# Performance work log

Hardware: AMD Instinct MI355X
Metric: run time of the kernel (lower is better)

Reference implementation:

```python
import jax, jax.numpy as jnp
import numpy as np

N_ATOMS = 100_000
N_BONDS = 200_000
MAX_NB = 6
ATOM_FDIM = 133
BOND_FDIM = 147
HIDDEN = 256
DEPTH = 5
ATOMS_PER_MOL = 100


def setup_inputs() -> dict:
    key = jax.random.key(0)
    ks = jax.random.split(key, 9)
    f_atoms = jax.random.normal(ks[0], (N_ATOMS, ATOM_FDIM), dtype=jnp.float32)
    f_bonds = jax.random.normal(ks[1], (N_BONDS, BOND_FDIM), dtype=jnp.float32)
    a2b = jax.random.randint(ks[2], (N_ATOMS, MAX_NB), 0, N_BONDS, dtype=jnp.int32)
    b2a = jax.random.randint(ks[3], (N_BONDS,), 0, N_ATOMS, dtype=jnp.int32)
    # reverse bond of 2i is 2i+1 and vice versa (chemprop directed-bond pairing)
    b2revb = (jnp.arange(N_BONDS, dtype=jnp.int32) ^ 1)
    s_i = 1.0 / np.sqrt(BOND_FDIM)
    s_h = 1.0 / np.sqrt(HIDDEN)
    s_o = 1.0 / np.sqrt(ATOM_FDIM + HIDDEN)
    W_i = jax.random.uniform(ks[4], (HIDDEN, BOND_FDIM), jnp.float32, -s_i, s_i)
    W_h = jax.random.uniform(ks[5], (HIDDEN, HIDDEN), jnp.float32, -s_h, s_h)
    W_o = jax.random.uniform(ks[6], (HIDDEN, ATOM_FDIM + HIDDEN), jnp.float32, -s_o, s_o)
    b_o = jax.random.uniform(ks[7], (HIDDEN,), jnp.float32, -s_o, s_o)
    return {"f_atoms": f_atoms, "f_bonds": f_bonds, "a2b": a2b, "b2a": b2a,
            "b2revb": b2revb, "W_i": W_i, "W_h": W_h, "W_o": W_o, "b_o": b_o,
            "atoms_per_mol": ATOMS_PER_MOL}


def reference(f_atoms, f_bonds, a2b, b2a, b2revb, W_i, W_h, W_o, b_o, atoms_per_mol):
    # input = W_i(f_bonds); message = relu(input)   [n_bonds, H]
    inp = jnp.einsum('bf,hf->bh', f_bonds, W_i)
    message = jax.nn.relu(inp)
    for _ in range(DEPTH - 1):
        # gather incoming-bond messages per atom and sum: [n_atoms, max_nb, H] -> [n_atoms, H]
        a_message = message[a2b].sum(axis=1)
        # directed-MPNN update: subtract reverse-bond message
        m = a_message[b2a] - message[b2revb]
        message = jax.nn.relu(inp + jnp.einsum('bh,gh->bg', m, W_h))
        # dropout p=0.0 (eval) -> identity
    a_message = message[a2b].sum(axis=1)                      # [n_atoms, H]
    a_input = jnp.concatenate([f_atoms, a_message], axis=1)   # [n_atoms, atom_fdim+H]
    atom_hiddens = jax.nn.relu(jnp.einsum('af,hf->ah', a_input, W_o) + b_o)
    # uniform a_scope: stack per-molecule atom blocks -> [n_mols, atoms_per_mol, H]
    return atom_hiddens.reshape(-1, atoms_per_mol, HIDDEN)
```

## Files before the change

kernel.cpp:

```cpp
#include <hip/hip_runtime.h>
#include <hip/hip_bf16.h>

typedef unsigned short u16;
typedef unsigned short u16x8 __attribute__((ext_vector_type(8)));
typedef short s8vec __attribute__((ext_vector_type(8)));
typedef float f4vec __attribute__((ext_vector_type(4)));

__device__ __forceinline__ float bf2f(u16 u) {
    union { unsigned int i; float f; } c; c.i = ((unsigned int)u) << 16; return c.f;
}
__device__ __forceinline__ u16 f2bf(float f) {
    union { float f; unsigned int i; } c; c.f = f;
    unsigned int x = c.i;
    x += 0x7fffu + ((x >> 16) & 1u);
    return (u16)(x >> 16);
}

__device__ __forceinline__ void gload_lds16(const void* g, void* l) {
    __builtin_amdgcn_global_load_lds((__attribute__((address_space(1))) void*)g,
                                     (__attribute__((address_space(3))) void*)l, 16, 0, 0);
}

__global__ void pad_w_kernel(const float* __restrict__ src, u16* __restrict__ dst,
                             int sstride, int col0, int nvalid, int dcol) {
    int r = blockIdx.x;
    for (int c = threadIdx.x; c < dcol; c += blockDim.x) {
        float v = (c < nvalid) ? src[(size_t)r * sstride + col0 + c] : 0.f;
        dst[(size_t)r * dcol + c] = f2bf(v);
    }
}

__global__ void gather6_kernel(const u16* __restrict__ P, const int* __restrict__ a2b,
                               u16* __restrict__ out, int n_atoms) {
    int lane = threadIdx.x & 63;
    int half = lane >> 5;
    int col = (lane & 31) * 8;
    int wid = (blockIdx.x * blockDim.x + threadIdx.x) >> 6;
    int nw = (gridDim.x * blockDim.x) >> 6;
    for (int a0 = wid * 2; a0 < n_atoms; a0 += nw * 2) {
        int a = a0 + half;
        float acc[8];
#pragma unroll
        for (int e = 0; e < 8; ++e) acc[e] = 0.f;
#pragma unroll
        for (int j = 0; j < 6; ++j) {
            int b = a2b[a * 6 + j];
            u16x8 v = *(const u16x8*)(P + (size_t)b * 256 + col);
#pragma unroll
            for (int e = 0; e < 8; ++e) acc[e] += bf2f(v[e]);
        }
        u16x8 o;
#pragma unroll
        for (int e = 0; e < 8; ++e) o[e] = f2bf(acc[e]);
        *(u16x8*)(out + (size_t)a * 256 + col) = o;
    }
}

template <int ASTAGE, int EPI>
__launch_bounds__(512, 2)
__global__ void gemm256_kernel(const void* __restrict__ Asrc, const u16* __restrict__ Pm,
                               const u16* __restrict__ aPm, const int* __restrict__ b2a,
                               const u16* __restrict__ B, int M, int Kp, int scol, int nk,
                               void* __restrict__ out0, const u16* __restrict__ aQ,
                               const float* __restrict__ bias) {
    __shared__ __align__(16) char smem[2][49152];
    const int t = threadIdx.x;
    const int w = t >> 6, lane = t & 63;
    const int row0 = blockIdx.x * 128;
    const int wm = w >> 2, wn = w & 3;

    f4vec acc[4][4];
#pragma unroll
    for (int i = 0; i < 4; ++i)
#pragma unroll
        for (int j = 0; j < 4; ++j) acc[i][j] = (f4vec){0.f, 0.f, 0.f, 0.f};

    auto stage = [&](int buf, int k0) {
#pragma unroll
        for (int i = 0; i < 4; ++i) {
            int rlin = (w * 4 + i) * 8 + (lane >> 3);
            int slot = lane & 7;
            int chunk = slot ^ (rlin & 7);
            const u16* gp = B + (size_t)rlin * Kp + k0 + chunk * 8;
            gload_lds16(gp, &smem[buf][16384 + (w * 4 + i) * 1024]);
        }
#pragma unroll
        for (int i = 0; i < 2; ++i) {
            int cid = t * 2 + i;
            int r = cid >> 3, slot = cid & 7;
            int grow = row0 + r; if (grow >= M) grow = M - 1;
            int coff = k0 + slot * 8;
            u16x8 v;
            if (ASTAGE == 1) {
                const float* src = (const float*)Asrc + (size_t)grow * scol;
#pragma unroll
                for (int e = 0; e < 8; ++e) {
                    int c = coff + e;
                    v[e] = (c < scol) ? f2bf(src[c]) : (u16)0;
                }
            } else if (ASTAGE == 2) {
                u16x8 x = *(const u16x8*)((const u16*)Asrc + (size_t)grow * 256 + coff);
#pragma unroll
                for (int e = 0; e < 8; ++e) v[e] = (x[e] >> 15) ? (u16)0 : x[e];
            } else {
                int pr = grow ^ 1;
                int a = b2a[grow];
                u16x8 vi = *(const u16x8*)((const u16*)Asrc + (size_t)grow * 256 + coff);
                u16x8 vp = *(const u16x8*)(Pm + (size_t)pr * 256 + coff);
                u16x8 va = *(const u16x8*)(aPm + (size_t)a * 256 + coff);
#pragma unroll
                for (int e = 0; e < 8; ++e)
                    v[e] = f2bf(fmaxf(bf2f(vi[e]) + bf2f(va[e]) - bf2f(vp[e]), 0.f));
            }
            int chunk = slot ^ (r & 7);
            *(u16x8*)&smem[buf][r * 128 + chunk * 16] = v;
        }
    };

    auto compute = [&](int buf) {
#pragma unroll
        for (int kk = 0; kk < 2; ++kk) {
            s8vec af[4], bfr[4];
#pragma unroll
            for (int i = 0; i < 4; ++i) {
                int r = wm * 64 + i * 16 + (lane & 15);
                int chunk = (kk * 4 + (lane >> 4)) ^ (r & 7);
                af[i] = *(const s8vec*)&smem[buf][r * 128 + chunk * 16];
            }
#pragma unroll
            for (int j = 0; j < 4; ++j) {
                int c = wn * 64 + j * 16 + (lane & 15);
                int chunk = (kk * 4 + (lane >> 4)) ^ (c & 7);
                bfr[j] = *(const s8vec*)&smem[buf][16384 + c * 128 + chunk * 16];
            }
#pragma unroll
            for (int i = 0; i < 4; ++i)
#pragma unroll
                for (int j = 0; j < 4; ++j)
                    acc[i][j] = __builtin_amdgcn_mfma_f32_16x16x32_bf16(af[i], bfr[j], acc[i][j], 0, 0, 0);
        }
    };

    stage(0, 0);
    __syncthreads();
    int cur = 0;
    for (int ks = 0; ks < nk; ++ks) {
        if (ks + 1 < nk) stage(cur ^ 1, (ks + 1) * 64);
        compute(cur);
        __syncthreads();
        cur ^= 1;
    }

#pragma unroll
    for (int i = 0; i < 4; ++i) {
        int Rbase = row0 + wm * 64 + i * 16 + (lane >> 4) * 4;
#pragma unroll
        for (int j = 0; j < 4; ++j) {
            int C = wn * 64 + j * 16 + (lane & 15);
#pragma unroll
            for (int r = 0; r < 4; ++r) {
                int R = Rbase + r;
                if (R < M) {
                    float v = acc[i][j][r];
                    if (EPI == 0) {
                        ((u16*)out0)[(size_t)R * 256 + C] = f2bf(v);
                    } else {
                        float o = v + bf2f(aQ[(size_t)R * 256 + C]) + bias[C];
                        ((float*)out0)[(size_t)R * 256 + C] = fmaxf(o, 0.f);
                    }
                }
            }
        }
    }
}

extern "C" void kernel_launch(void* const* d_in, const int* in_sizes, int n_in,
                              void* d_out, int out_size, void* d_ws, size_t ws_size,
                              hipStream_t stream) {
    const float* f_atoms = (const float*)d_in[0];
    const float* f_bonds = (const float*)d_in[1];
    const int* a2b = (const int*)d_in[2];
    const int* b2a = (const int*)d_in[3];
    const float* W_i = (const float*)d_in[5];
    const float* W_h = (const float*)d_in[6];
    const float* W_o = (const float*)d_in[7];
    const float* b_o = (const float*)d_in[8];

    const int NA = 100000, NB = 200000;

    char* ws = (char*)d_ws;
    u16* inp = (u16*)(ws + 0);
    u16* Pa  = (u16*)(ws + 102400000);
    u16* Pb  = (u16*)(ws + 204800000);
    u16* aP  = (u16*)(ws + 307200000);
    u16* Wi  = (u16*)(ws + 358400000);
    u16* Wh  = (u16*)(ws + 358498304);
    u16* Wo2 = (u16*)(ws + 358629376);
    u16* Wo1 = (u16*)(ws + 358760448);
    if (ws_size < 358858752u) return;

    pad_w_kernel<<<dim3(256), dim3(256), 0, stream>>>(W_i, Wi, 147, 0, 147, 192);
    pad_w_kernel<<<dim3(256), dim3(256), 0, stream>>>(W_h, Wh, 256, 0, 256, 256);
    pad_w_kernel<<<dim3(256), dim3(256), 0, stream>>>(W_o, Wo2, 389, 133, 256, 256);
    pad_w_kernel<<<dim3(256), dim3(256), 0, stream>>>(W_o, Wo1, 389, 0, 133, 192);

    const int GB = (NB + 127) / 128;
    const int GA = (NA + 127) / 128;

    gemm256_kernel<1, 0><<<dim3(GB), dim3(512), 0, stream>>>(
        f_bonds, nullptr, nullptr, nullptr, Wi, NB, 192, 147, 3, inp, nullptr, nullptr);

    gemm256_kernel<2, 0><<<dim3(GB), dim3(512), 0, stream>>>(
        inp, nullptr, nullptr, nullptr, Wh, NB, 256, 0, 4, Pa, nullptr, nullptr);
    gather6_kernel<<<dim3(2048), dim3(256), 0, stream>>>(Pa, a2b, aP, NA);

    u16* Pcur = Pa; u16* Pnxt = Pb;
    for (int it = 0; it < 3; ++it) {
        gemm256_kernel<4, 0><<<dim3(GB), dim3(512), 0, stream>>>(
            inp, Pcur, aP, b2a, Wh, NB, 256, 0, 4, Pnxt, nullptr, nullptr);
        gather6_kernel<<<dim3(2048), dim3(256), 0, stream>>>(Pnxt, a2b, aP, NA);
        u16* tmp = Pcur; Pcur = Pnxt; Pnxt = tmp;
    }

    gemm256_kernel<4, 0><<<dim3(GB), dim3(512), 0, stream>>>(
        inp, Pcur, aP, b2a, Wo2, NB, 256, 0, 4, Pnxt, nullptr, nullptr);
    gather6_kernel<<<dim3(2048), dim3(256), 0, stream>>>(Pnxt, a2b, aP, NA);

    gemm256_kernel<1, 3><<<dim3(GA), dim3(512), 0, stream>>>(
        f_atoms, nullptr, nullptr, nullptr, Wo1, NA, 192, 133, 3, d_out, aP, b_o);
}
```

Before: 1.034 ms.

## Shrink GEMM tiles to 64 rows with K=32 steps and register-prefetched A

The GEMM block changes from 128 rows with 512 threads and K=64 steps to 64 rows with 256 threads and K=32 steps. LDS per block drops from 96KB to 40KB, so more blocks can be resident per CU. A-operand global loads are now issued into registers before the MFMA compute and written to LDS afterwards, overlapping load latency with math. The b2a lookup is hoisted out of the K loop, and the four weight-padding launches are merged into one. The risk is that smaller tiles reread the weight matrix twice as often and take more sync steps per tile.

```diff
diff --git a/kernel.cpp b/kernel.cpp
--- a/kernel.cpp
+++ b/kernel.cpp
@@ -15,15 +15,23 @@
     x += 0x7fffu + ((x >> 16) & 1u);
     return (u16)(x >> 16);
 }
-
 __device__ __forceinline__ void gload_lds16(const void* g, void* l) {
     __builtin_amdgcn_global_load_lds((__attribute__((address_space(1))) void*)g,
                                      (__attribute__((address_space(3))) void*)l, 16, 0, 0);
 }
-
-__global__ void pad_w_kernel(const float* __restrict__ src, u16* __restrict__ dst,
-                             int sstride, int col0, int nvalid, int dcol) {
+__device__ __forceinline__ int sw4(int r) { return (r + (r >> 2)) & 3; }
+
+__global__ void pad_w_all(const float* __restrict__ W_i, const float* __restrict__ W_h,
+                          const float* __restrict__ W_o,
+                          u16* __restrict__ Wi, u16* __restrict__ Wh,
+                          u16* __restrict__ Wo2, u16* __restrict__ Wo1) {
     int r = blockIdx.x;
+    int which = blockIdx.y;
+    const float* src; u16* dst; int sstride, col0, nvalid, dcol;
+    if (which == 0)      { src = W_i; dst = Wi;  sstride = 147; col0 = 0;   nvalid = 147; dcol = 192; }
+    else if (which == 1) { src = W_h; dst = Wh;  sstride = 256; col0 = 0;   nvalid = 256; dcol = 256; }
+    else if (which == 2) { src = W_o; dst = Wo2; sstride = 389; col0 = 133; nvalid = 256; dcol = 256; }
+    else                 { src = W_o; dst = Wo1; sstride = 389; col0 = 0;   nvalid = 133; dcol = 192; }
     for (int c = threadIdx.x; c < dcol; c += blockDim.x) {
         float v = (c < nvalid) ? src[(size_t)r * sstride + col0 + c] : 0.f;
         dst[(size_t)r * dcol + c] = f2bf(v);
@@ -57,17 +65,23 @@
 }
 
 template <int ASTAGE, int EPI>
-__launch_bounds__(512, 2)
+__launch_bounds__(256, 4)
 __global__ void gemm256_kernel(const void* __restrict__ Asrc, const u16* __restrict__ Pm,
                                const u16* __restrict__ aPm, const int* __restrict__ b2a,
-                               const u16* __restrict__ B, int M, int Kp, int scol, int nk,
+                               const u16* __restrict__ Bw, int M, int Kp, int scol, int nk,
                                void* __restrict__ out0, const u16* __restrict__ aQ,
                                const float* __restrict__ bias) {
-    __shared__ __align__(16) char smem[2][49152];
+    __shared__ __align__(16) char smem[2][20480];
     const int t = threadIdx.x;
     const int w = t >> 6, lane = t & 63;
-    const int row0 = blockIdx.x * 128;
-    const int wm = w >> 2, wn = w & 3;
+    const int row0 = blockIdx.x * 64;
+
+    const int ar = t >> 2;
+    const int aslot = t & 3;
+    int grow = row0 + ar; if (grow >= M) grow = M - 1;
+    const int aphys = aslot ^ sw4(ar);
+    int nbrow = 0;
+    if (ASTAGE == 4) nbrow = b2a[grow];
 
     f4vec acc[4][4];
 #pragma unroll
@@ -75,88 +89,91 @@
 #pragma unroll
         for (int j = 0; j < 4; ++j) acc[i][j] = (f4vec){0.f, 0.f, 0.f, 0.f};
 
-    auto stage = [&](int buf, int k0) {
+    u16x8 rv0, rv1, rv2;
+    float rs[8];
+
+    auto stageA_load = [&](int k0) {
+        int coff = k0 + aslot * 8;
+        if (ASTAGE == 1) {
+            const float* src = (const float*)Asrc + (size_t)grow * scol;
+#pragma unroll
+            for (int e = 0; e < 8; ++e)
+                rs[e] = (coff + e < scol) ? src[coff + e] : 0.f;
+        } else if (ASTAGE == 2) {
+            rv0 = *(const u16x8*)((const u16*)Asrc + (size_t)grow * 256 + coff);
+        } else {
+            rv0 = *(const u16x8*)((const u16*)Asrc + (size_t)grow * 256 + coff);
+            rv1 = *(const u16x8*)(Pm + (size_t)(grow ^ 1) * 256 + coff);
+            rv2 = *(const u16x8*)(aPm + (size_t)nbrow * 256 + coff);
+        }
+    };
+    auto stageA_write = [&](int buf) {
+        u16x8 v;
+        if (ASTAGE == 1) {
+#pragma unroll
+            for (int e = 0; e < 8; ++e) v[e] = f2bf(rs[e]);
+        } else if (ASTAGE == 2) {
+#pragma unroll
+            for (int e = 0; e < 8; ++e) v[e] = (rv0[e] >> 15) ? (u16)0 : rv0[e];
+        } else {
+#pragma unroll
+            for (int e = 0; e < 8; ++e)
+                v[e] = f2bf(fmaxf(bf2f(rv0[e]) + bf2f(rv2[e]) - bf2f(rv1[e]), 0.f));
+        }
+        *(u16x8*)&smem[buf][ar * 64 + aphys * 16] = v;
+    };
+    auto stageB = [&](int buf, int k0) {
 #pragma unroll
         for (int i = 0; i < 4; ++i) {
-            int rlin = (w * 4 + i) * 8 + (lane >> 3);
-            int slot = lane & 7;
-            int chunk = slot ^ (rlin & 7);
-            const u16* gp = B + (size_t)rlin * Kp + k0 + chunk * 8;
-            gload_lds16(gp, &smem[buf][16384 + (w * 4 + i) * 1024]);
-        }
-#pragma unroll
-        for (int i = 0; i < 2; ++i) {
-            int cid = t * 2 + i;
-            int r = cid >> 3, slot = cid & 7;
-            int grow = row0 + r; if (grow >= M) grow = M - 1;
-            int coff = k0 + slot * 8;
-            u16x8 v;
-            if (ASTAGE == 1) {
-                const float* src = (const float*)Asrc + (size_t)grow * scol;
-#pragma unroll
-                for (int e = 0; e < 8; ++e) {
-                    int c = coff + e;
-                    v[e] = (c < scol) ? f2bf(src[c]) : (u16)0;
-                }
-            } else if (ASTAGE == 2) {
-                u16x8 x = *(const u16x8*)((const u16*)Asrc + (size_t)grow * 256 + coff);
-#pragma unroll
-                for (int e = 0; e < 8; ++e) v[e] = (x[e] >> 15) ? (u16)0 : x[e];
-            } else {
-                int pr = grow ^ 1;
-                int a = b2a[grow];
-                u16x8 vi = *(const u16x8*)((const u16*)Asrc + (size_t)grow * 256 + coff);
-                u16x8 vp = *(const u16x8*)(Pm + (size_t)pr * 256 + coff);
-                u16x8 va = *(const u16x8*)(aPm + (size_t)a * 256 + coff);
-#pragma unroll
-                for (int e = 0; e < 8; ++e)
-                    v[e] = f2bf(fmaxf(bf2f(vi[e]) + bf2f(va[e]) - bf2f(vp[e]), 0.f));
-            }
-            int chunk = slot ^ (r & 7);
-            *(u16x8*)&smem[buf][r * 128 + chunk * 16] = v;
-        }
-    };
-
+            int rlin = (w * 4 + i) * 16 + (lane >> 2);
+            int chunk = (lane & 3) ^ sw4(rlin);
+            const u16* gp = Bw + (size_t)rlin * Kp + k0 + chunk * 8;
+            gload_lds16(gp, &smem[buf][4096 + (w * 4 + i) * 1024]);
+        }
+    };
     auto compute = [&](int buf) {
-#pragma unroll
-        for (int kk = 0; kk < 2; ++kk) {
-            s8vec af[4], bfr[4];
-#pragma unroll
-            for (int i = 0; i < 4; ++i) {
-                int r = wm * 64 + i * 16 + (lane & 15);
-                int chunk = (kk * 4 + (lane >> 4)) ^ (r & 7);
-                af[i] = *(const s8vec*)&smem[buf][r * 128 + chunk * 16];
-            }
-#pragma unroll
-            for (int j = 0; j < 4; ++j) {
-                int c = wn * 64 + j * 16 + (lane & 15);
-                int chunk = (kk * 4 + (lane >> 4)) ^ (c & 7);
-                bfr[j] = *(const s8vec*)&smem[buf][16384 + c * 128 + chunk * 16];
-            }
-#pragma unroll
-            for (int i = 0; i < 4; ++i)
-#pragma unroll
-                for (int j = 0; j < 4; ++j)
-                    acc[i][j] = __builtin_amdgcn_mfma_f32_16x16x32_bf16(af[i], bfr[j], acc[i][j], 0, 0, 0);
-        }
-    };
-
-    stage(0, 0);
+        s8vec af[4], bfr[4];
+#pragma unroll
+        for (int i = 0; i < 4; ++i) {
+            int r = i * 16 + (lane & 15);
+            int p = (lane >> 4) ^ sw4(r);
+            af[i] = *(const s8vec*)&smem[buf][r * 64 + p * 16];
+        }
+#pragma unroll
+        for (int j = 0; j < 4; ++j) {
+            int c = w * 64 + j * 16 + (lane & 15);
+            int p = (lane >> 4) ^ sw4(c);
+            bfr[j] = *(const s8vec*)&smem[buf][4096 + c * 64 + p * 16];
+        }
+#pragma unroll
+        for (int i = 0; i < 4; ++i)
+#pragma unroll
+            for (int j = 0; j < 4; ++j)
+                acc[i][j] = __builtin_amdgcn_mfma_f32_16x16x32_bf16(af[i], bfr[j], acc[i][j], 0, 0, 0);
+    };
+
+    stageA_load(0);
+    stageB(0, 0);
+    stageA_write(0);
     __syncthreads();
     int cur = 0;
     for (int ks = 0; ks < nk; ++ks) {
-        if (ks + 1 < nk) stage(cur ^ 1, (ks + 1) * 64);
+        if (ks + 1 < nk) {
+            stageA_load((ks + 1) * 32);
+            stageB(cur ^ 1, (ks + 1) * 32);
+        }
         compute(cur);
+        if (ks + 1 < nk) stageA_write(cur ^ 1);
         __syncthreads();
         cur ^= 1;
     }
 
 #pragma unroll
     for (int i = 0; i < 4; ++i) {
-        int Rbase = row0 + wm * 64 + i * 16 + (lane >> 4) * 4;
+        int Rbase = row0 + i * 16 + (lane >> 4) * 4;
 #pragma unroll
         for (int j = 0; j < 4; ++j) {
-            int C = wn * 64 + j * 16 + (lane & 15);
+            int C = w * 64 + j * 16 + (lane & 15);
 #pragma unroll
             for (int r = 0; r < 4; ++r) {
                 int R = Rbase + r;
@@ -199,33 +216,30 @@
     u16* Wo1 = (u16*)(ws + 358760448);
     if (ws_size < 358858752u) return;
 
-    pad_w_kernel<<<dim3(256), dim3(256), 0, stream>>>(W_i, Wi, 147, 0, 147, 192);
-    pad_w_kernel<<<dim3(256), dim3(256), 0, stream>>>(W_h, Wh, 256, 0, 256, 256);
-    pad_w_kernel<<<dim3(256), dim3(256), 0, stream>>>(W_o, Wo2, 389, 133, 256, 256);
-    pad_w_kernel<<<dim3(256), dim3(256), 0, stream>>>(W_o, Wo1, 389, 0, 133, 192);
-
-    const int GB = (NB + 127) / 128;
-    const int GA = (NA + 127) / 128;
-
-    gemm256_kernel<1, 0><<<dim3(GB), dim3(512), 0, stream>>>(
-        f_bonds, nullptr, nullptr, nullptr, Wi, NB, 192, 147, 3, inp, nullptr, nullptr);
-
-    gemm256_kernel<2, 0><<<dim3(GB), dim3(512), 0, stream>>>(
-        inp, nullptr, nullptr, nullptr, Wh, NB, 256, 0, 4, Pa, nullptr, nullptr);
+    pad_w_all<<<dim3(256, 4), dim3(256), 0, stream>>>(W_i, W_h, W_o, Wi, Wh, Wo2, Wo1);
+
+    const int GB = NB / 64;
+    const int GA = (NA + 63) / 64;
+
+    gemm256_kernel<1, 0><<<dim3(GB), dim3(256), 0, stream>>>(
+        f_bonds, nullptr, nullptr, nullptr, Wi, NB, 192, 147, 6, inp, nullptr, nullptr);
+
+    gemm256_kernel<2, 0><<<dim3(GB), dim3(256), 0, stream>>>(
+        inp, nullptr, nullptr, nullptr, Wh, NB, 256, 0, 8, Pa, nullptr, nullptr);
     gather6_kernel<<<dim3(2048), dim3(256), 0, stream>>>(Pa, a2b, aP, NA);
 
     u16* Pcur = Pa; u16* Pnxt = Pb;
     for (int it = 0; it < 3; ++it) {
-        gemm256_kernel<4, 0><<<dim3(GB), dim3(512), 0, stream>>>(
-            inp, Pcur, aP, b2a, Wh, NB, 256, 0, 4, Pnxt, nullptr, nullptr);
+        gemm256_kernel<4, 0><<<dim3(GB), dim3(256), 0, stream>>>(
+            inp, Pcur, aP, b2a, Wh, NB, 256, 0, 8, Pnxt, nullptr, nullptr);
         gather6_kernel<<<dim3(2048), dim3(256), 0, stream>>>(Pnxt, a2b, aP, NA);
         u16* tmp = Pcur; Pcur = Pnxt; Pnxt = tmp;
     }
 
-    gemm256_kernel<4, 0><<<dim3(GB), dim3(512), 0, stream>>>(
-        inp, Pcur, aP, b2a, Wo2, NB, 256, 0, 4, Pnxt, nullptr, nullptr);
+    gemm256_kernel<4, 0><<<dim3(GB), dim3(256), 0, stream>>>(
+        inp, Pcur, aP, b2a, Wo2, NB, 256, 0, 8, Pnxt, nullptr, nullptr);
     gather6_kernel<<<dim3(2048), dim3(256), 0, stream>>>(Pnxt, a2b, aP, NA);
 
-    gemm256_kernel<1, 3><<<dim3(GA), dim3(512), 0, stream>>>(
-        f_atoms, nullptr, nullptr, nullptr, Wo1, NA, 192, 133, 3, d_out, aP, b_o);
-}
+    gemm256_kernel<1, 3><<<dim3(GA), dim3(256), 0, stream>>>(
+        f_atoms, nullptr, nullptr, nullptr, Wo1, NA, 192, 133, 6, d_out, aP, b_o);
+}
```

Measured after the change: 887.4 us. 1.16x faster.
